# Performance work log

Hardware: AMD Instinct MI355X
Metric: run time of the kernel (lower is better)

Reference implementation:

```python
import jax, jax.numpy as jnp
import numpy as np
import math

B, IN, D, H, DEPTH, E, K = 16384, 128, 512, 8, 3, 8, 2
FF, EH = 4 * D, 256          # ffn width = 4*d_model; expert hidden fixed at 256 in source
EPSILON = 0.1                # forward() default epsilon (exploration mixing)
LN_EPS = 1e-5


def _ln(x, w, b):
    m = x.mean(-1, keepdims=True)
    v = x.var(-1, keepdims=True)  # biased variance, matching nn.LayerNorm
    return (x - m) / jnp.sqrt(v + LN_EPS) * w + b


def setup_inputs() -> dict:
    key = jax.random.key(0)
    ks = jax.random.split(key, 16)
    s = 0.02
    rn = lambda k, shape: jax.random.normal(k, shape, jnp.float32) * s
    return dict(
        x=jax.random.normal(ks[0], (B, IN), jnp.float32),
        embed_w=rn(ks[1], (IN, D)), embed_b=jnp.zeros((D,), jnp.float32),
        ln1_w=jnp.ones((DEPTH, D), jnp.float32), ln1_b=jnp.zeros((DEPTH, D), jnp.float32),
        inproj_w=rn(ks[2], (DEPTH, 3 * D, D)), inproj_b=jnp.zeros((DEPTH, 3 * D), jnp.float32),
        outproj_w=rn(ks[3], (DEPTH, D, D)), outproj_b=jnp.zeros((DEPTH, D), jnp.float32),
        ln2_w=jnp.ones((DEPTH, D), jnp.float32), ln2_b=jnp.zeros((DEPTH, D), jnp.float32),
        ffn_w1=rn(ks[4], (DEPTH, D, FF)), ffn_b1=jnp.zeros((DEPTH, FF), jnp.float32),
        ffn_w2=rn(ks[5], (DEPTH, FF, D)), ffn_b2=jnp.zeros((DEPTH, D), jnp.float32),
        router_w=rn(ks[6], (D, E)), router_b=jnp.zeros((E,), jnp.float32),
        exp_w1=rn(ks[7], (E, D, EH)), exp_b1=jnp.zeros((E, EH), jnp.float32),
        exp_w2=rn(ks[8], (E, EH, D)), exp_b2=jnp.zeros((E, D), jnp.float32),
        head_ln_w=jnp.ones((D,), jnp.float32), head_ln_b=jnp.zeros((D,), jnp.float32),
        head_w=rn(ks[9], (D, 1)), head_b=jnp.zeros((1,), jnp.float32),
    )


def reference(x, embed_w, embed_b, ln1_w, ln1_b, inproj_w, inproj_b,
              outproj_w, outproj_b, ln2_w, ln2_b, ffn_w1, ffn_b1, ffn_w2, ffn_b2,
              router_w, router_b, exp_w1, exp_b1, exp_w2, exp_b2,
              head_ln_w, head_ln_b, head_w, head_b):
    h = x @ embed_w + embed_b                       # [B, D]; unsqueeze(1) -> seq_len == 1
    for l in range(DEPTH):
        g = _ln(h, ln1_w[l], ln1_b[l])
        qkv = g @ inproj_w[l].T + inproj_b[l]       # [B, 3D]
        # seq_len == 1: softmax over the single key is exactly 1, so attn(h,h,h) == out_proj(V)
        v = qkv[:, 2 * D:]
        a = v @ outproj_w[l].T + outproj_b[l]
        h = h + a
        g = _ln(h, ln2_w[l], ln2_b[l])
        h = h + jax.nn.gelu(g @ ffn_w1[l] + ffn_b1[l], approximate=False) @ ffn_w2[l] + ffn_b2[l]
    z = h                                           # squeeze(1)

    # WaggleGate
    logits = z @ router_w + router_b                # [B, E]
    probs = jax.nn.softmax(logits, axis=-1)
    probs = (1.0 - EPSILON) * probs + EPSILON / E
    wts, idx = jax.lax.top_k(probs, K)              # [B, K]
    load = probs.mean(0)
    aux = (load * jnp.log(load * E + 1e-9)).sum() / math.log(E + 1e-9)

    # dense all-expert compute + sparse top-k combine (same math as per-sample dispatch)
    hmid = jax.nn.gelu(jnp.einsum('bd,edh->ebh', z, exp_w1) + exp_b1[:, None, :], approximate=False)
    eo = jnp.einsum('ebh,ehd->ebd', hmid, exp_w2) + exp_b2[:, None, :]   # [E, B, D]
    gate = jnp.zeros((z.shape[0], E), z.dtype).at[
        jnp.arange(z.shape[0])[:, None], idx].add(wts)                    # [B, E]
    moe = jnp.einsum('be,ebd->bd', gate, eo)

    z = z + moe
    logit = (_ln(z, head_ln_w, head_ln_b) @ head_w + head_b)[:, 0]       # [B]
    return logit, aux
```

## Files before the change

### kernel.cpp

```cpp
#include <hip/hip_runtime.h>
#include <hip/hip_bf16.h>

#define B_TOK 16384
#define IN_DIM 128
#define D_DIM 512
#define DEPTH 3
#define NEXP 8
#define FF_DIM 2048
#define EH_DIM 256
#define MAXSLOT 34816
#define MAXT256 136
#define NHBLK 64

typedef __attribute__((ext_vector_type(8))) __bf16 bf16x8;
typedef __attribute__((ext_vector_type(4))) float f32x4;
typedef __attribute__((ext_vector_type(4))) unsigned short u16x4;
typedef __attribute__((ext_vector_type(8))) unsigned short u16x8;

__device__ __forceinline__ unsigned short f2bf(float f){
    unsigned int u = __float_as_uint(f);
    u += 0x7fffu + ((u >> 16) & 1u);
    return (unsigned short)(u >> 16);
}
__device__ __forceinline__ float bf2f(unsigned short u){
    return __uint_as_float(((unsigned int)u) << 16);
}
__device__ __forceinline__ float geluf(float x){
    return 0.5f * x * (1.0f + erff(x * 0.70710678118654752f));
}
__device__ __forceinline__ void gload_lds16(const void* g, void* l){
    __builtin_amdgcn_global_load_lds((const __attribute__((address_space(1))) unsigned int*)g,
                                     (__attribute__((address_space(3))) unsigned int*)l,
                                     16, 0, 0);
}
__device__ __forceinline__ int xcd_swizzle(int orig, int nwg){
    const int q = nwg >> 3, r = nwg & 7;
    const int xcd = orig & 7;
    const int idx = orig >> 3;
    return (xcd < r ? xcd*(q+1) : r*(q+1) + (xcd-r)*q) + idx;
}
__device__ __forceinline__ void wgbar(){
    asm volatile("" ::: "memory");
    __builtin_amdgcn_s_barrier();
    asm volatile("" ::: "memory");
}

__global__ void zero_kernel(int* a, int na, int* b, int nb){
    const int i = blockIdx.x * blockDim.x + threadIdx.x;
    if (i < na) a[i] = 0;
    if (i < nb) b[i] = 0;
}

struct ConvSeg { const float* src; unsigned short* dst; int n4; };
struct ConvArgs { ConvSeg seg[2]; };

__global__ void convert_kernel(ConvArgs a){
    const int stride = gridDim.x * blockDim.x;
    const int tid = blockIdx.x * blockDim.x + threadIdx.x;
    for (int s = 0; s < 2; ++s){
        const f32x4* src = (const f32x4*)a.seg[s].src;
        u16x4* dst = (u16x4*)a.seg[s].dst;
        const int n4 = a.seg[s].n4;
        for (int i = tid; i < n4; i += stride){
            f32x4 v = src[i];
            u16x4 o;
            o[0] = f2bf(v[0]); o[1] = f2bf(v[1]); o[2] = f2bf(v[2]); o[3] = f2bf(v[3]);
            dst[i] = o;
        }
    }
}

struct TSeg { const float* src; unsigned short* dst; int K; int N; int tileStart; };
struct TArgs { TSeg seg[26]; };

__global__ void transpose_kernel(TArgs a){
    __shared__ float t[32][33];
    const int tile = blockIdx.x;
    int s = 0;
    #pragma unroll 1
    while (s < 25 && tile >= a.seg[s+1].tileStart) ++s;
    const TSeg sg = a.seg[s];
    const int local = tile - sg.tileStart;
    const int tilesN = sg.N >> 5;
    const int k0 = (local / tilesN) << 5;
    const int n0 = (local % tilesN) << 5;
    const int tx = threadIdx.x & 31;
    const int ty = threadIdx.x >> 5;
    #pragma unroll
    for (int j = 0; j < 4; ++j)
        t[ty + j*8][tx] = sg.src[(size_t)(k0 + ty + j*8) * sg.N + n0 + tx];
    __syncthreads();
    #pragma unroll
    for (int j = 0; j < 4; ++j){
        const int n = ty + j*8;
        sg.dst[(size_t)(n0 + n) * sg.K + k0 + tx] = f2bf(t[tx][n]);
    }
}

__global__ void foldb_kernel(const float* __restrict__ outproj_w, const float* __restrict__ outproj_b,
                             const float* __restrict__ inproj_b, float* __restrict__ bfold){
    const int l = blockIdx.x, n = threadIdx.x;
    const float* Wo = outproj_w + ((size_t)l*D_DIM + n)*D_DIM;
    const float* bv = inproj_b + l*3*D_DIM + 2*D_DIM;
    float acc = outproj_b[l*D_DIM + n];
    for (int j = 0; j < D_DIM; ++j) acc += Wo[j]*bv[j];
    bfold[l*D_DIM + n] = acc;
}

#define EPI_BF16 0
#define EPI_F32_BIAS 2

template<int EPI>
__global__ void __launch_bounds__(256, 2)
gemm_bt(const unsigned short* __restrict__ A, const unsigned short* __restrict__ Bt,
        const float* __restrict__ bias, void* __restrict__ out, int NB, int N, int K)
{
    __shared__ unsigned short sh[32768];
    const int nwg = gridDim.x;
    const int wg  = xcd_swizzle(blockIdx.x, nwg);
    const int bn  = wg % NB;
    const int bm  = wg / NB;

    const int tid  = threadIdx.x;
    const int lane = tid & 63;
    const int wave = tid >> 6;
    const int wm = (wave >> 1) << 6;
    const int wn = (wave & 1) << 6;

    f32x4 acc[4][4] = {};

    const unsigned short* Abase = A + (size_t)bm * 128 * K;
    const unsigned short* Bbase = Bt + (size_t)bn * 128 * K;
    const int soff = tid * 16;

    auto STAGE = [&](int b, int kt){
        char* Ab = (char*)(sh + b*16384);
        char* Bb = (char*)(sh + b*16384 + 8192);
        #pragma unroll
        for (int s = 0; s < 4; ++s){
            const int off = s*4096 + soff;
            const int row = off >> 7, colb = off & 127;
            gload_lds16((const char*)(Abase + (size_t)row*K + kt) + colb, Ab + off);
        }
        #pragma unroll
        for (int s = 0; s < 4; ++s){
            const int off = s*4096 + soff;
            const int row = off >> 7, colb = off & 127;
            gload_lds16((const char*)(Bbase + (size_t)row*K + kt) + colb, Bb + off);
        }
    };
    auto COMPUTE = [&](int b){
        const unsigned short* Ab = sh + b*16384;
        const unsigned short* Bb = sh + b*16384 + 8192;
        #pragma unroll
        for (int ks = 0; ks < 2; ++ks){
            const int k0 = ks*32 + ((lane>>4)<<3);
            bf16x8 af[4], bfr[4];
            #pragma unroll
            for (int i=0;i<4;i++) af[i]  = *(const bf16x8*)&Ab[(wm + i*16 + (lane&15))*64 + k0];
            #pragma unroll
            for (int j=0;j<4;j++) bfr[j] = *(const bf16x8*)&Bb[(wn + j*16 + (lane&15))*64 + k0];
            #pragma unroll
            for (int i=0;i<4;i++)
                #pragma unroll
                for (int j=0;j<4;j++)
                    acc[i][j] = __builtin_amdgcn_mfma_f32_16x16x32_bf16(af[i], bfr[j], acc[i][j], 0, 0, 0);
        }
    };

    STAGE(0, 0);
    __syncthreads();
    const int nk = K >> 6;
    int cur = 0;
    for (int i = 0; i < nk; ++i){
        if (i + 1 < nk) STAGE(cur ^ 1, (i + 1) << 6);
        COMPUTE(cur);
        __syncthreads();
        cur ^= 1;
    }

    const int r0 = ((lane>>4)<<2);
    const int cc = lane & 15;

    if (EPI == EPI_F32_BIAS){
        #pragma unroll
        for (int j=0;j<4;j++){
            const int col = bn*128 + wn + j*16 + cc;
            const float bv = bias[col];
            #pragma unroll
            for (int i=0;i<4;i++)
                #pragma unroll
                for (int r=0;r<4;r++){
                    const int row = bm*128 + wm + i*16 + r0 + r;
                    ((float*)out)[(size_t)row * N + col] = acc[i][j][r] + bv;
                }
        }
    } else {
        unsigned short* Ct = sh;
        float bcol[4];
        #pragma unroll
        for (int j=0;j<4;j++) bcol[j] = bias[bn*128 + wn + j*16 + cc];
        #pragma unroll
        for (int i=0;i<4;i++)
            #pragma unroll
            for (int r=0;r<4;r++){
                const int rl = wm + i*16 + r0 + r;
                #pragma unroll
                for (int j=0;j<4;j++)
                    Ct[rl*128 + wn + j*16 + cc] = f2bf(acc[i][j][r] + bcol[j]);
            }
        __syncthreads();
        const int orow = tid >> 4;
        const int ocol = (tid & 15) * 8;
        unsigned short* op = (unsigned short*)out;
        #pragma unroll
        for (int p = 0; p < 8; ++p){
            const int row = p*16 + orow;
            *(u16x4*)(&op[(size_t)(bm*128 + row)*N + bn*128 + ocol])     = *(u16x4*)&Ct[row*128 + ocol];
            *(u16x4*)(&op[(size_t)(bm*128 + row)*N + bn*128 + ocol + 4]) = *(u16x4*)&Ct[row*128 + ocol + 4];
        }
    }
}

#define G_GELU_BF16 0
#define G_F32_RESID 1
#define G_GATED_BF16 2

template<int EPI, int MOE, int INDIRECT>
__global__ void __launch_bounds__(512, 2)
gemm256(const unsigned short* __restrict__ A, const unsigned short* __restrict__ BtG,
        const float* __restrict__ biasG, const float* __restrict__ resid,
        const int* __restrict__ tok, const int* __restrict__ offs,
        int wstride, int bstride, const float* __restrict__ gslot,
        void* __restrict__ out, int NB, int N, int K)
{
    __shared__ __align__(16) char sh[147456];
    const int nwg = gridDim.x;
    const int wg  = xcd_swizzle(blockIdx.x, nwg);
    const int bn  = wg % NB;
    const int bm  = wg / NB;
    const int m0  = bm * 256;

    const unsigned short* Bt = BtG;
    const float* bias = biasG;
    if (MOE){
        if (m0 >= offs[8]) return;
        int e = 0;
        #pragma unroll 1
        while (offs[e+1] <= m0) ++e;
        Bt   += (size_t)e * wstride;
        bias += (size_t)e * bstride;
    }

    const int tid = threadIdx.x, lane = tid & 63, wave = tid >> 6;
    const int wm = (wave >> 1) * 64;
    const int wn = (wave & 1) * 64;

    const int srow = wave*16 + (lane >> 3);
    const int scol = ((lane & 7) ^ (lane >> 3)) * 8;
    const unsigned short* aptr[2][2];
    #pragma unroll
    for (int u = 0; u < 2; ++u)
        #pragma unroll
        for (int l = 0; l < 2; ++l){
            const int r = u*128 + srow + l*8;
            const int gr = INDIRECT ? tok[m0 + r] : (m0 + r);
            aptr[u][l] = A + (size_t)gr * K + scol;
        }
    const unsigned short* bptr[2];
    #pragma unroll
    for (int l = 0; l < 2; ++l)
        bptr[l] = Bt + (size_t)(bn*128 + srow + l*8) * K + scol;
    const int sdst = wave*2048 + lane*16;

    int aoff[2], boff[2];
    #pragma unroll
    for (int ks = 0; ks < 2; ++ks){
        const int ch = (((ks<<2) + (lane>>4)) ^ (lane & 7)) << 4;
        aoff[ks] = (wm + (lane & 15))*128 + ch;
        boff[ks] = (wn + (lane & 15))*128 + ch;
    }

    f32x4 acc[4][4] = {};
    bf16x8 bfr[4][2];

    auto STA = [&](int buf, int kt){
        #pragma unroll
        for (int u = 0; u < 2; ++u)
            #pragma unroll
            for (int l = 0; l < 2; ++l)
                gload_lds16(aptr[u][l] + kt, sh + buf*32768 + u*16384 + l*1024 + sdst);
    };
    auto STB = [&](int buf, int kt){
        #pragma unroll
        for (int l = 0; l < 2; ++l)
            gload_lds16(bptr[l] + kt, sh + 98304 + buf*16384 + l*1024 + sdst);
    };
    auto RDB = [&](int buf){
        #pragma unroll
        for (int nf = 0; nf < 4; ++nf)
            #pragma unroll
            for (int ks = 0; ks < 2; ++ks)
                bfr[nf][ks] = *(const bf16x8*)(sh + 98304 + buf*16384 + nf*2048 + boff[ks]);
    };

    STA(0, 0);  STB(0, 0);
    STA(1, 64); STB(1, 64);
    asm volatile("s_waitcnt vmcnt(6)" ::: "memory");
    wgbar();

    const int nk = K >> 6;
    int c0 = 0;
    for (int t = 0; t < nk; ++t){
        const bool f = (t + 2 < nk);
        int c2 = c0 + 2; if (c2 >= 3) c2 -= 3;
        bf16x8 af[2][2];

        RDB(c0);
        #pragma unroll
        for (int m2 = 0; m2 < 2; ++m2)
            #pragma unroll
            for (int ks = 0; ks < 2; ++ks)
                af[m2][ks] = *(const bf16x8*)(sh + c0*32768 + (0+m2)*2048 + aoff[ks]);
        if (f){
            const int kt2 = (t + 2) << 6;
            STA(c2, kt2);
            STB(c2, kt2);
        }
        __builtin_amdgcn_s_setprio(1);
        #pragma unroll
        for (int m2 = 0; m2 < 2; ++m2)
            #pragma unroll
            for (int nf = 0; nf < 4; ++nf)
                #pragma unroll
                for (int ks = 0; ks < 2; ++ks)
                    acc[0+m2][nf] = __builtin_amdgcn_mfma_f32_16x16x32_bf16(af[m2][ks], bfr[nf][ks], acc[0+m2][nf], 0,0,0);
        __builtin_amdgcn_s_setprio(0);
        wgbar();

        #pragma unroll
        for (int m2 = 0; m2 < 2; ++m2)
            #pragma unroll
            for (int ks = 0; ks < 2; ++ks)
                af[m2][ks] = *(const bf16x8*)(sh + c0*32768 + (2+m2)*2048 + aoff[ks]);
        __builtin_amdgcn_s_setprio(1);
        #pragma unroll
        for (int m2 = 0; m2 < 2; ++m2)
            #pragma unroll
            for (int nf = 0; nf < 4; ++nf)
                #pragma unroll
                for (int ks = 0; ks < 2; ++ks)
                    acc[2+m2][nf] = __builtin_amdgcn_mfma_f32_16x16x32_bf16(af[m2][ks], bfr[nf][ks], acc[2+m2][nf], 0,0,0);
        __builtin_amdgcn_s_setprio(0);
        if (f) asm volatile("s_waitcnt vmcnt(6)" ::: "memory");
        else   asm volatile("s_waitcnt vmcnt(0)" ::: "memory");
        wgbar();

        ++c0; if (c0 >= 3) c0 -= 3;
    }

    const int r4 = (lane >> 4) * 4;
    const int cc = lane & 15;
    if (EPI == G_F32_RESID){
        #pragma unroll
        for (int nf = 0; nf < 4; ++nf){
            const int col = bn*128 + wn + nf*16 + cc;
            const float bv = bias[col];
            #pragma unroll
            for (int mf = 0; mf < 4; ++mf)
                #pragma unroll
                for (int r = 0; r < 4; ++r){
                    const int row = m0 + wm + mf*16 + r4 + r;
                    const size_t idx = (size_t)row * N + col;
                    ((float*)out)[idx] = resid[idx] + acc[mf][nf][r] + bv;
                }
        }
    } else {
        unsigned short* ct = (unsigned short*)sh;
        #pragma unroll
        for (int nf = 0; nf < 4; ++nf){
            const float bv = bias[bn*128 + wn + nf*16 + cc];
            #pragma unroll
            for (int mf = 0; mf < 4; ++mf)
                #pragma unroll
                for (int r = 0; r < 4; ++r){
                    const int row = wm + mf*16 + r4 + r;
                    float v = acc[mf][nf][r] + bv;
                    if (EPI == G_GELU_BF16) v = geluf(v);
                    else                    v *= gslot[m0 + row];
                    ct[row*128 + wn + nf*16 + cc] = f2bf(v);
                }
        }
        __syncthreads();
        unsigned short* op = (unsigned short*)out;
        #pragma unroll
        for (int p = 0; p < 8; ++p){
            const int uidx = p*512 + tid;
            const int row = uidx >> 4;
            const int cu  = uidx & 15;
            *(u16x8*)(op + (size_t)(m0 + row)*N + bn*128 + cu*8) =
                *(const u16x8*)(ct + row*128 + cu*8);
        }
    }
}

__global__ void ln_kernel(const float* __restrict__ x, const float* __restrict__ w,
                          const float* __restrict__ b, unsigned short* __restrict__ out)
{
    const int lane = threadIdx.x & 63;
    const int wave = threadIdx.x >> 6;
    const int row  = blockIdx.x * 4 + wave;
    const float* xr = x + (size_t)row * D_DIM;
    f32x4 v0 = *(const f32x4*)(xr + lane*8);
    f32x4 v1 = *(const f32x4*)(xr + lane*8 + 4);
    float s  = v0[0]+v0[1]+v0[2]+v0[3] + v1[0]+v1[1]+v1[2]+v1[3];
    float s2 = v0[0]*v0[0]+v0[1]*v0[1]+v0[2]*v0[2]+v0[3]*v0[3]
             + v1[0]*v1[0]+v1[1]*v1[1]+v1[2]*v1[2]+v1[3]*v1[3];
    #pragma unroll
    for (int o = 32; o > 0; o >>= 1){ s += __shfl_xor(s, o); s2 += __shfl_xor(s2, o); }
    const float mean = s * (1.0f/512.0f);
    const float var  = s2 * (1.0f/512.0f) - mean*mean;
    const float inv  = 1.0f / sqrtf(var + 1e-5f);
    const int k = lane*8;
    u16x4 o0, o1;
    #pragma unroll
    for (int j=0;j<4;j++) o0[j] = f2bf((v0[j]-mean)*inv*w[k+j]   + b[k+j]);
    #pragma unroll
    for (int j=0;j<4;j++) o1[j] = f2bf((v1[j]-mean)*inv*w[k+4+j] + b[k+4+j]);
    *(u16x4*)(out + (size_t)row*D_DIM + k)     = o0;
    *(u16x4*)(out + (size_t)row*D_DIM + k + 4) = o1;
}

__global__ void router_kernel(const float* __restrict__ z, const float* __restrict__ rw,
                              const float* __restrict__ rb, unsigned short* __restrict__ zbf,
                              int2* __restrict__ idx2, float2* __restrict__ wts2,
                              float* __restrict__ bsums)
{
    __shared__ float ps[4][8];
    const int lane = threadIdx.x & 63;
    const int wave = threadIdx.x >> 6;
    const int row  = blockIdx.x * 4 + wave;
    const float* zr = z + (size_t)row * D_DIM;
    f32x4 z0 = *(const f32x4*)(zr + lane*8);
    f32x4 z1 = *(const f32x4*)(zr + lane*8 + 4);
    {
        u16x4 o0, o1;
        #pragma unroll
        for (int j=0;j<4;j++){ o0[j] = f2bf(z0[j]); o1[j] = f2bf(z1[j]); }
        *(u16x4*)(zbf + (size_t)row*D_DIM + lane*8)     = o0;
        *(u16x4*)(zbf + (size_t)row*D_DIM + lane*8 + 4) = o1;
    }
    float acc[8] = {0,0,0,0,0,0,0,0};
    #pragma unroll
    for (int j = 0; j < 8; ++j){
        const float zv = (j < 4) ? z0[j] : z1[j-4];
        const float* wr = rw + (size_t)(lane*8 + j) * 8;
        f32x4 w0 = *(const f32x4*)wr;
        f32x4 w1 = *(const f32x4*)(wr + 4);
        acc[0] += zv*w0[0]; acc[1] += zv*w0[1]; acc[2] += zv*w0[2]; acc[3] += zv*w0[3];
        acc[4] += zv*w1[0]; acc[5] += zv*w1[1]; acc[6] += zv*w1[2]; acc[7] += zv*w1[3];
    }
    #pragma unroll
    for (int o = 32; o > 0; o >>= 1){
        #pragma unroll
        for (int e = 0; e < 8; ++e) acc[e] += __shfl_xor(acc[e], o);
    }
    if (lane == 0){
        float p[8]; float mx = -1e30f;
        #pragma unroll
        for (int e=0;e<8;e++){ p[e] = acc[e] + rb[e]; mx = fmaxf(mx, p[e]); }
        float se = 0.f;
        #pragma unroll
        for (int e=0;e<8;e++){ p[e] = expf(p[e]-mx); se += p[e]; }
        const float sc = 0.9f / se;
        #pragma unroll
        for (int e=0;e<8;e++) p[e] = p[e]*sc + 0.0125f;
        int i1 = 0;
        #pragma unroll
        for (int e=1;e<8;e++) if (p[e] > p[i1]) i1 = e;
        int i2 = (i1 == 0) ? 1 : 0;
        for (int e=i2+1;e<8;e++) if (e != i1 && p[e] > p[i2]) i2 = e;
        idx2[row] = make_int2(i1, i2);
        wts2[row] = make_float2(p[i1], p[i2]);
        #pragma unroll
        for (int e=0;e<8;e++) ps[wave][e] = p[e];
    }
    __syncthreads();
    if (threadIdx.x < 8){
        bsums[blockIdx.x*8 + threadIdx.x] =
            ps[0][threadIdx.x] + ps[1][threadIdx.x] + ps[2][threadIdx.x] + ps[3][threadIdx.x];
    }
}

__global__ void hist_kernel(const int2* __restrict__ idx2, int* __restrict__ blockHist){
    __shared__ int hc[8];
    if (threadIdx.x < 8) hc[threadIdx.x] = 0;
    __syncthreads();
    const int t = blockIdx.x * 256 + threadIdx.x;
    const int2 ii = idx2[t];
    atomicAdd(&hc[ii.x], 1);
    atomicAdd(&hc[ii.y], 1);
    __syncthreads();
    if (threadIdx.x < 8) blockHist[blockIdx.x*8 + threadIdx.x] = hc[threadIdx.x];
}

__global__ void scan_kernel(const int* __restrict__ blockHist, int* __restrict__ offs,
                            int* __restrict__ baseArr){
    if (threadIdx.x == 0){
        int counts[8];
        #pragma unroll
        for (int e=0;e<8;e++) counts[e] = 0;
        for (int b=0;b<NHBLK;b++)
            #pragma unroll
            for (int e=0;e<8;e++) counts[e] += blockHist[b*8+e];
        int o = 0; offs[0] = 0;
        int start[8];
        #pragma unroll
        for (int e=0;e<8;e++){ start[e] = o; o += (counts[e]+255)&~255; offs[e+1] = o; }
        for (int e=0;e<8;e++){
            int cur = start[e];
            for (int b=0;b<NHBLK;b++){ baseArr[b*8+e] = cur; cur += blockHist[b*8+e]; }
        }
    }
}

__global__ void assign_kernel(const int2* __restrict__ idx2, const float2* __restrict__ wts2,
                              const int* __restrict__ baseArr, int2* __restrict__ slot_map,
                              float* __restrict__ gslot, int* __restrict__ tok)
{
    __shared__ int cur[8];
    if (threadIdx.x < 8) cur[threadIdx.x] = 0;
    __syncthreads();
    const int t = blockIdx.x * 256 + threadIdx.x;
    const int2 ii = idx2[t];
    const float2 ww = wts2[t];
    const int r1 = atomicAdd(&cur[ii.x], 1);
    const int r2 = atomicAdd(&cur[ii.y], 1);
    const int s1 = baseArr[blockIdx.x*8 + ii.x] + r1;
    const int s2 = baseArr[blockIdx.x*8 + ii.y] + r2;
    slot_map[t] = make_int2(s1, s2);
    gslot[s1] = ww.x; gslot[s2] = ww.y;
    tok[s1] = t; tok[s2] = t;
}

__global__ void aux_kernel(const float* __restrict__ bsums, float* __restrict__ out_aux)
{
    __shared__ float part[256];
    const int t = threadIdx.x;
    const int e = t & 7, chunk = t >> 3;
    float s = 0.f;
    for (int blk = chunk*128; blk < chunk*128 + 128; ++blk) s += bsums[blk*8 + e];
    part[t] = s;
    __syncthreads();
    if (t < 8){
        float tot = 0.f;
        for (int c = 0; c < 32; ++c) tot += part[c*8 + t];
        part[t] = tot;
    }
    __syncthreads();
    if (t == 0){
        float aux = 0.f;
        for (int e2 = 0; e2 < 8; ++e2){
            float load = part[e2] * (1.0f/16384.0f);
            aux += load * logf(load * 8.0f + 1e-9f);
        }
        out_aux[0] = aux / 2.0794415416798357f;
    }
}

__global__ void head_kernel(const float* __restrict__ h, const unsigned short* __restrict__ eog,
                            const int2* __restrict__ slot_map,
                            const float* __restrict__ w, const float* __restrict__ b,
                            const float* __restrict__ hw, const float* __restrict__ hb,
                            float* __restrict__ out)
{
    const int lane = threadIdx.x & 63;
    const int wave = threadIdx.x >> 6;
    const int row  = blockIdx.x * 4 + wave;
    const int2 sm = slot_map[row];
    const float* zr = h + (size_t)row * D_DIM;
    f32x4 v0 = *(const f32x4*)(zr + lane*8);
    f32x4 v1 = *(const f32x4*)(zr + lane*8 + 4);
    u16x8 e1 = *(const u16x8*)(eog + (size_t)sm.x * D_DIM + lane*8);
    u16x8 e2 = *(const u16x8*)(eog + (size_t)sm.y * D_DIM + lane*8);
    #pragma unroll
    for (int j=0;j<4;j++){ v0[j] += bf2f(e1[j]) + bf2f(e2[j]); }
    #pragma unroll
    for (int j=0;j<4;j++){ v1[j] += bf2f(e1[4+j]) + bf2f(e2[4+j]); }
    float s  = v0[0]+v0[1]+v0[2]+v0[3] + v1[0]+v1[1]+v1[2]+v1[3];
    float s2 = v0[0]*v0[0]+v0[1]*v0[1]+v0[2]*v0[2]+v0[3]*v0[3]
             + v1[0]*v1[0]+v1[1]*v1[1]+v1[2]*v1[2]+v1[3]*v1[3];
    #pragma unroll
    for (int o = 32; o > 0; o >>= 1){ s += __shfl_xor(s, o); s2 += __shfl_xor(s2, o); }
    const float mean = s * (1.0f/512.0f);
    const float var  = s2 * (1.0f/512.0f) - mean*mean;
    const float inv  = 1.0f / sqrtf(var + 1e-5f);
    const int k = lane*8;
    float dot = 0.f;
    #pragma unroll
    for (int j=0;j<4;j++) dot += ((v0[j]-mean)*inv*w[k+j]   + b[k+j])   * hw[k+j];
    #pragma unroll
    for (int j=0;j<4;j++) dot += ((v1[j]-mean)*inv*w[k+4+j] + b[k+4+j]) * hw[k+4+j];
    #pragma unroll
    for (int o = 32; o > 0; o >>= 1) dot += __shfl_xor(dot, o);
    if (lane == 0) out[row] = dot + hb[0];
}

extern "C" void kernel_launch(void* const* d_in, const int* in_sizes, int n_in,
                              void* d_out, int out_size, void* d_ws, size_t ws_size,
                              hipStream_t stream)
{
    (void)in_sizes; (void)n_in; (void)out_size; (void)ws_size;
    const float* x         = (const float*)d_in[0];
    const float* embed_w   = (const float*)d_in[1];
    const float* embed_b   = (const float*)d_in[2];
    const float* ln1_w     = (const float*)d_in[3];
    const float* ln1_b     = (const float*)d_in[4];
    const float* inproj_w  = (const float*)d_in[5];
    const float* inproj_b  = (const float*)d_in[6];
    const float* outproj_w = (const float*)d_in[7];
    const float* outproj_b = (const float*)d_in[8];
    const float* ln2_w     = (const float*)d_in[9];
    const float* ln2_b     = (const float*)d_in[10];
    const float* ffn_w1    = (const float*)d_in[11];
    const float* ffn_b1    = (const float*)d_in[12];
    const float* ffn_w2    = (const float*)d_in[13];
    const float* ffn_b2    = (const float*)d_in[14];
    const float* router_w  = (const float*)d_in[15];
    const float* router_b  = (const float*)d_in[16];
    const float* exp_w1    = (const float*)d_in[17];
    const float* exp_b1    = (const float*)d_in[18];
    const float* exp_w2    = (const float*)d_in[19];
    const float* exp_b2    = (const float*)d_in[20];
    const float* head_ln_w = (const float*)d_in[21];
    const float* head_ln_b = (const float*)d_in[22];
    const float* head_w    = (const float*)d_in[23];
    const float* head_b    = (const float*)d_in[24];

    char* ws = (char*)d_ws;
    unsigned short* xbf   = (unsigned short*)(ws + 0);
    unsigned short* ebf   = (unsigned short*)(ws + 4194304);
    unsigned short* wobf  = (unsigned short*)(ws + 4325376);
    unsigned short* wvtbf = (unsigned short*)(ws + 5898240);
    unsigned short* wfold = (unsigned short*)(ws + 7471104);
    unsigned short* w1t   = (unsigned short*)(ws + 9043968);
    unsigned short* w2t   = (unsigned short*)(ws + 15335424);
    unsigned short* e1t   = (unsigned short*)(ws + 21626880);
    unsigned short* e2t   = (unsigned short*)(ws + 23724032);
    float*          h     = (float*)(ws + 25821184);
    unsigned short* gbf   = (unsigned short*)(ws + 59375616);
    unsigned short* ubf   = (unsigned short*)(ws + 76152832);
    unsigned short* hmidg = ubf;
    unsigned short* eog   = (unsigned short*)(ws + 93978624);
    char* MISC = ws + 143261696;
    int*    offs     = (int*)(MISC + 0);
    float*  zbias    = (float*)(MISC + 256);
    float*  bfold    = (float*)(MISC + 2304);
    int2*   idx2     = (int2*)(MISC + 8448);
    float2* wts2     = (float2*)(MISC + 139520);
    int2*   slot_map = (int2*)(MISC + 270592);
    float*  gslot    = (float*)(MISC + 401664);
    int*    tok      = (int*)(MISC + 544768);
    float*  bsums    = (float*)(MISC + 684032);
    int*    blockHist= (int*)(MISC + 815104);
    int*    baseArr  = (int*)(MISC + 817152);
    unsigned short* zbf = gbf;
    float* out = (float*)d_out;

    zero_kernel<<<(MAXSLOT + 255)/256, 256, 0, stream>>>((int*)zbias, 512, tok, MAXSLOT);

    ConvArgs ca;
    ca.seg[0] = { x, xbf, B_TOK*IN_DIM/4 };
    ca.seg[1] = { outproj_w, wobf, DEPTH*D_DIM*D_DIM/4 };
    convert_kernel<<<1024, 256, 0, stream>>>(ca);

    TArgs ta;
    int tcur = 0, ti = 0;
    ta.seg[ti] = { embed_w, ebf, IN_DIM, D_DIM, tcur };
    tcur += (IN_DIM/32)*(D_DIM/32); ++ti;
    for (int l = 0; l < DEPTH; ++l){
        ta.seg[ti] = { ffn_w1 + (size_t)l*D_DIM*FF_DIM, w1t + (size_t)l*FF_DIM*D_DIM, D_DIM, FF_DIM, tcur };
        tcur += (D_DIM/32)*(FF_DIM/32); ++ti;
    }
    for (int l = 0; l < DEPTH; ++l){
        ta.seg[ti] = { ffn_w2 + (size_t)l*FF_DIM*D_DIM, w2t + (size_t)l*D_DIM*FF_DIM, FF_DIM, D_DIM, tcur };
        tcur += (FF_DIM/32)*(D_DIM/32); ++ti;
    }
    for (int e = 0; e < NEXP; ++e){
        ta.seg[ti] = { exp_w1 + (size_t)e*D_DIM*EH_DIM, e1t + (size_t)e*EH_DIM*D_DIM, D_DIM, EH_DIM, tcur };
        tcur += (D_DIM/32)*(EH_DIM/32); ++ti;
    }
    for (int e = 0; e < NEXP; ++e){
        ta.seg[ti] = { exp_w2 + (size_t)e*EH_DIM*D_DIM, e2t + (size_t)e*D_DIM*EH_DIM, EH_DIM, D_DIM, tcur };
        tcur += (EH_DIM/32)*(D_DIM/32); ++ti;
    }
    for (int l = 0; l < DEPTH; ++l){
        ta.seg[ti] = { inproj_w + (size_t)l*3*D_DIM*D_DIM + 2*D_DIM*D_DIM,
                       wvtbf + (size_t)l*D_DIM*D_DIM, D_DIM, D_DIM, tcur };
        tcur += (D_DIM/32)*(D_DIM/32); ++ti;
    }
    transpose_kernel<<<tcur, 256, 0, stream>>>(ta);

    foldb_kernel<<<DEPTH, D_DIM, 0, stream>>>(outproj_w, outproj_b, inproj_b, bfold);

    for (int l = 0; l < DEPTH; ++l){
        gemm_bt<EPI_BF16><<<16, 256, 0, stream>>>(
            wobf + (size_t)l*D_DIM*D_DIM, wvtbf + (size_t)l*D_DIM*D_DIM,
            zbias, wfold + (size_t)l*D_DIM*D_DIM, 4, D_DIM, D_DIM);
    }

    gemm_bt<EPI_F32_BIAS><<<(D_DIM/128)*(B_TOK/128), 256, 0, stream>>>(
        xbf, ebf, embed_b, h, D_DIM/128, D_DIM, IN_DIM);

    for (int l = 0; l < DEPTH; ++l){
        ln_kernel<<<B_TOK/4, 256, 0, stream>>>(h, ln1_w + l*D_DIM, ln1_b + l*D_DIM, gbf);
        gemm256<G_F32_RESID,0,0><<<(B_TOK/256)*(D_DIM/128), 512, 0, stream>>>(
            gbf, wfold + (size_t)l*D_DIM*D_DIM, bfold + l*D_DIM, h,
            nullptr, nullptr, 0, 0, nullptr, h, D_DIM/128, D_DIM, D_DIM);
        ln_kernel<<<B_TOK/4, 256, 0, stream>>>(h, ln2_w + l*D_DIM, ln2_b + l*D_DIM, gbf);
        gemm256<G_GELU_BF16,0,0><<<(B_TOK/256)*(FF_DIM/128), 512, 0, stream>>>(
            gbf, w1t + (size_t)l*FF_DIM*D_DIM, ffn_b1 + l*FF_DIM, nullptr,
            nullptr, nullptr, 0, 0, nullptr, ubf, FF_DIM/128, FF_DIM, D_DIM);
        gemm256<G_F32_RESID,0,0><<<(B_TOK/256)*(D_DIM/128), 512, 0, stream>>>(
            ubf, w2t + (size_t)l*D_DIM*FF_DIM, ffn_b2 + l*D_DIM, h,
            nullptr, nullptr, 0, 0, nullptr, h, D_DIM/128, D_DIM, FF_DIM);
    }

    router_kernel<<<B_TOK/4, 256, 0, stream>>>(h, router_w, router_b, zbf, idx2, wts2, bsums);
    aux_kernel<<<1, 256, 0, stream>>>(bsums, out + B_TOK);
    hist_kernel<<<NHBLK, 256, 0, stream>>>(idx2, blockHist);
    scan_kernel<<<1, 64, 0, stream>>>(blockHist, offs, baseArr);
    assign_kernel<<<B_TOK/256, 256, 0, stream>>>(idx2, wts2, baseArr, slot_map, gslot, tok);

    gemm256<G_GELU_BF16,1,1><<<MAXT256*(EH_DIM/128), 512, 0, stream>>>(
        zbf, e1t, exp_b1, nullptr, tok, offs, EH_DIM*D_DIM, EH_DIM, nullptr,
        hmidg, EH_DIM/128, EH_DIM, D_DIM);
    gemm256<G_GATED_BF16,1,0><<<MAXT256*(D_DIM/128), 512, 0, stream>>>(
        hmidg, e2t, exp_b2, nullptr, nullptr, offs, D_DIM*EH_DIM, D_DIM, gslot,
        eog, D_DIM/128, D_DIM, EH_DIM);

    head_kernel<<<B_TOK/4, 256, 0, stream>>>(h, eog, slot_map, head_ln_w, head_ln_b, head_w, head_b, out);
}
```

Baseline: 673.9 us.

## Store residual stream in bf16, add 256x256 FFN1 GEMM, tanh GELU, simplify pipeline

Stores the residual stream h as bf16 instead of fp32. This halves the traffic of the LN, residual-GEMM, router and head kernels, and lets the expert GEMM read h directly without a separate bf16 copy. Adds a 256x256-tile GEMM for the FFN up-projection to raise data reuse, and replaces erf GELU with a clamped tanh approximation. The gemm256 main loop is also reverted from a 3-stage prefetch with explicit waitcnt and setprio to a plain 2-stage double buffer. Together these trade accuracy (bf16 residual accumulation and approximate GELU) and possibly some pipelining efficiency for less memory traffic and cheaper math.

```diff
diff --git a/kernel.cpp b/kernel.cpp
--- a/kernel.cpp
+++ b/kernel.cpp
@@ -26,7 +26,12 @@
     return __uint_as_float(((unsigned int)u) << 16);
 }
 __device__ __forceinline__ float geluf(float x){
-    return 0.5f * x * (1.0f + erff(x * 0.70710678118654752f));
+    float x2 = x * x;
+    float y  = x * (0.79788456080287f + 0.03567740814183f * x2);
+    y = fminf(fmaxf(y, -15.0f), 15.0f);
+    float e = __expf(2.0f * y);
+    float th = 1.0f - 2.0f / (e + 1.0f);
+    return 0.5f * x * (1.0f + th);
 }
 __device__ __forceinline__ void gload_lds16(const void* g, void* l){
     __builtin_amdgcn_global_load_lds((const __attribute__((address_space(1))) unsigned int*)g,
@@ -38,11 +43,6 @@
     const int xcd = orig & 7;
     const int idx = orig >> 3;
     return (xcd < r ? xcd*(q+1) : r*(q+1) + (xcd-r)*q) + idx;
-}
-__device__ __forceinline__ void wgbar(){
-    asm volatile("" ::: "memory");
-    __builtin_amdgcn_s_barrier();
-    asm volatile("" ::: "memory");
 }
 
 __global__ void zero_kernel(int* a, int na, int* b, int nb){
@@ -107,13 +107,9 @@
     bfold[l*D_DIM + n] = acc;
 }
 
-#define EPI_BF16 0
-#define EPI_F32_BIAS 2
-
-template<int EPI>
 __global__ void __launch_bounds__(256, 2)
 gemm_bt(const unsigned short* __restrict__ A, const unsigned short* __restrict__ Bt,
-        const float* __restrict__ bias, void* __restrict__ out, int NB, int N, int K)
+        const float* __restrict__ bias, unsigned short* __restrict__ out, int NB, int N, int K)
 {
     __shared__ unsigned short sh[32768];
     const int nwg = gridDim.x;
@@ -181,58 +177,148 @@
 
     const int r0 = ((lane>>4)<<2);
     const int cc = lane & 15;
-
-    if (EPI == EPI_F32_BIAS){
-        #pragma unroll
-        for (int j=0;j<4;j++){
-            const int col = bn*128 + wn + j*16 + cc;
-            const float bv = bias[col];
-            #pragma unroll
-            for (int i=0;i<4;i++)
+    unsigned short* Ct = sh;
+    float bcol[4];
+    #pragma unroll
+    for (int j=0;j<4;j++) bcol[j] = bias[bn*128 + wn + j*16 + cc];
+    #pragma unroll
+    for (int i=0;i<4;i++)
+        #pragma unroll
+        for (int r=0;r<4;r++){
+            const int rl = wm + i*16 + r0 + r;
+            #pragma unroll
+            for (int j=0;j<4;j++)
+                Ct[rl*128 + wn + j*16 + cc] = f2bf(acc[i][j][r] + bcol[j]);
+        }
+    __syncthreads();
+    const int orow = tid >> 4;
+    const int ocol = (tid & 15) * 8;
+    #pragma unroll
+    for (int p = 0; p < 8; ++p){
+        const int row = p*16 + orow;
+        *(u16x8*)(&out[(size_t)(bm*128 + row)*N + bn*128 + ocol]) = *(u16x8*)&Ct[row*128 + ocol];
+    }
+}
+
+__global__ void __launch_bounds__(512, 2)
+gemm256sq(const unsigned short* __restrict__ A, const unsigned short* __restrict__ Bt,
+          const float* __restrict__ bias, unsigned short* __restrict__ out,
+          int NB, int N, int K)
+{
+    __shared__ __align__(16) char sh[131072];
+    const int nwg = gridDim.x;
+    const int wg  = xcd_swizzle(blockIdx.x, nwg);
+    const int bn  = wg % NB;
+    const int bm  = wg / NB;
+    const int m0  = bm * 256;
+    const int n0  = bn * 256;
+
+    const int tid = threadIdx.x, lane = tid & 63, wave = tid >> 6;
+    const int wr = wave >> 2;
+    const int wc = wave & 3;
+
+    const int srow = wave*16 + (lane >> 3);
+    const int scol = ((lane & 7) ^ (lane >> 3)) * 8;
+    const unsigned short* aptr[2][2];
+    const unsigned short* bptr[2][2];
+    #pragma unroll
+    for (int u = 0; u < 2; ++u)
+        #pragma unroll
+        for (int l = 0; l < 2; ++l){
+            aptr[u][l] = A  + (size_t)(m0 + u*128 + srow + l*8) * K + scol;
+            bptr[u][l] = Bt + (size_t)(n0 + u*128 + srow + l*8) * K + scol;
+        }
+    const int sdst = wave*2048 + lane*16;
+
+    int ch[2];
+    #pragma unroll
+    for (int ks = 0; ks < 2; ++ks)
+        ch[ks] = ((((ks<<2) + (lane>>4)) ^ (lane & 7)) << 4);
+    const int arow = wr*128 + (lane & 15);
+    const int brow = wc*64  + (lane & 15);
+
+    f32x4 acc[8][4] = {};
+
+    auto STAGE = [&](int buf, int kt){
+        #pragma unroll
+        for (int u = 0; u < 2; ++u)
+            #pragma unroll
+            for (int l = 0; l < 2; ++l)
+                gload_lds16(aptr[u][l] + kt, sh + buf*32768 + u*16384 + l*1024 + sdst);
+        #pragma unroll
+        for (int u = 0; u < 2; ++u)
+            #pragma unroll
+            for (int l = 0; l < 2; ++l)
+                gload_lds16(bptr[u][l] + kt, sh + 65536 + buf*32768 + u*16384 + l*1024 + sdst);
+    };
+    auto COMPUTE = [&](int buf){
+        bf16x8 bfr[4][2];
+        #pragma unroll
+        for (int nf = 0; nf < 4; ++nf)
+            #pragma unroll
+            for (int ks = 0; ks < 2; ++ks)
+                bfr[nf][ks] = *(const bf16x8*)(sh + 65536 + buf*32768 + (brow + nf*16)*128 + ch[ks]);
+        #pragma unroll
+        for (int mf = 0; mf < 8; ++mf){
+            bf16x8 af[2];
+            #pragma unroll
+            for (int ks = 0; ks < 2; ++ks)
+                af[ks] = *(const bf16x8*)(sh + buf*32768 + (arow + mf*16)*128 + ch[ks]);
+            #pragma unroll
+            for (int nf = 0; nf < 4; ++nf)
                 #pragma unroll
-                for (int r=0;r<4;r++){
-                    const int row = bm*128 + wm + i*16 + r0 + r;
-                    ((float*)out)[(size_t)row * N + col] = acc[i][j][r] + bv;
-                }
-        }
-    } else {
-        unsigned short* Ct = sh;
-        float bcol[4];
-        #pragma unroll
-        for (int j=0;j<4;j++) bcol[j] = bias[bn*128 + wn + j*16 + cc];
-        #pragma unroll
-        for (int i=0;i<4;i++)
-            #pragma unroll
-            for (int r=0;r<4;r++){
-                const int rl = wm + i*16 + r0 + r;
-                #pragma unroll
-                for (int j=0;j<4;j++)
-                    Ct[rl*128 + wn + j*16 + cc] = f2bf(acc[i][j][r] + bcol[j]);
+                for (int ks = 0; ks < 2; ++ks)
+                    acc[mf][nf] = __builtin_amdgcn_mfma_f32_16x16x32_bf16(af[ks], bfr[nf][ks], acc[mf][nf], 0,0,0);
+        }
+    };
+
+    STAGE(0, 0);
+    __syncthreads();
+    const int nk = K >> 6;
+    int cur = 0;
+    for (int i = 0; i < nk; ++i){
+        if (i + 1 < nk) STAGE(cur ^ 1, (i + 1) << 6);
+        COMPUTE(cur);
+        __syncthreads();
+        cur ^= 1;
+    }
+
+    unsigned short* Ct = (unsigned short*)sh;
+    const int r4 = (lane >> 4) * 4;
+    const int cc = lane & 15;
+    #pragma unroll
+    for (int nf = 0; nf < 4; ++nf){
+        const int col = wc*64 + nf*16 + cc;
+        const float bv = bias[n0 + col];
+        #pragma unroll
+        for (int mf = 0; mf < 8; ++mf)
+            #pragma unroll
+            for (int r = 0; r < 4; ++r){
+                const int row = wr*128 + mf*16 + r4 + r;
+                Ct[row*256 + col] = f2bf(geluf(acc[mf][nf][r] + bv));
             }
-        __syncthreads();
-        const int orow = tid >> 4;
-        const int ocol = (tid & 15) * 8;
-        unsigned short* op = (unsigned short*)out;
-        #pragma unroll
-        for (int p = 0; p < 8; ++p){
-            const int row = p*16 + orow;
-            *(u16x4*)(&op[(size_t)(bm*128 + row)*N + bn*128 + ocol])     = *(u16x4*)&Ct[row*128 + ocol];
-            *(u16x4*)(&op[(size_t)(bm*128 + row)*N + bn*128 + ocol + 4]) = *(u16x4*)&Ct[row*128 + ocol + 4];
-        }
+    }
+    __syncthreads();
+    #pragma unroll
+    for (int p = 0; p < 16; ++p){
+        const int uidx = p*512 + tid;
+        const int row = uidx >> 5;
+        const int cu  = uidx & 31;
+        *(u16x8*)(out + (size_t)(m0 + row)*N + n0 + cu*8) = *(const u16x8*)(Ct + row*256 + cu*8);
     }
 }
 
 #define G_GELU_BF16 0
-#define G_F32_RESID 1
+#define G_BF16_RESID 1
 #define G_GATED_BF16 2
 
 template<int EPI, int MOE, int INDIRECT>
 __global__ void __launch_bounds__(512, 2)
 gemm256(const unsigned short* __restrict__ A, const unsigned short* __restrict__ BtG,
-        const float* __restrict__ biasG, const float* __restrict__ resid,
+        const float* __restrict__ biasG, const unsigned short* __restrict__ resid,
         const int* __restrict__ tok, const int* __restrict__ offs,
         int wstride, int bstride, const float* __restrict__ gslot,
-        void* __restrict__ out, int NB, int N, int K)
+        unsigned short* __restrict__ out, int NB, int N, int K)
 {
     __shared__ __align__(16) char sh[147456];
     const int nwg = gridDim.x;
@@ -282,98 +368,77 @@
     }
 
     f32x4 acc[4][4] = {};
-    bf16x8 bfr[4][2];
-
-    auto STA = [&](int buf, int kt){
+
+    auto STAGE = [&](int buf, int kt){
         #pragma unroll
         for (int u = 0; u < 2; ++u)
             #pragma unroll
             for (int l = 0; l < 2; ++l)
                 gload_lds16(aptr[u][l] + kt, sh + buf*32768 + u*16384 + l*1024 + sdst);
-    };
-    auto STB = [&](int buf, int kt){
         #pragma unroll
         for (int l = 0; l < 2; ++l)
             gload_lds16(bptr[l] + kt, sh + 98304 + buf*16384 + l*1024 + sdst);
     };
-    auto RDB = [&](int buf){
+    auto COMPUTE = [&](int buf){
+        bf16x8 bfr[4][2];
         #pragma unroll
         for (int nf = 0; nf < 4; ++nf)
             #pragma unroll
             for (int ks = 0; ks < 2; ++ks)
                 bfr[nf][ks] = *(const bf16x8*)(sh + 98304 + buf*16384 + nf*2048 + boff[ks]);
-    };
-
-    STA(0, 0);  STB(0, 0);
-    STA(1, 64); STB(1, 64);
-    asm volatile("s_waitcnt vmcnt(6)" ::: "memory");
-    wgbar();
-
-    const int nk = K >> 6;
-    int c0 = 0;
-    for (int t = 0; t < nk; ++t){
-        const bool f = (t + 2 < nk);
-        int c2 = c0 + 2; if (c2 >= 3) c2 -= 3;
-        bf16x8 af[2][2];
-
-        RDB(c0);
-        #pragma unroll
-        for (int m2 = 0; m2 < 2; ++m2)
+        #pragma unroll
+        for (int mf = 0; mf < 4; ++mf){
+            bf16x8 af[2];
             #pragma unroll
             for (int ks = 0; ks < 2; ++ks)
-                af[m2][ks] = *(const bf16x8*)(sh + c0*32768 + (0+m2)*2048 + aoff[ks]);
-        if (f){
-            const int kt2 = (t + 2) << 6;
-            STA(c2, kt2);
-            STB(c2, kt2);
-        }
-        __builtin_amdgcn_s_setprio(1);
-        #pragma unroll
-        for (int m2 = 0; m2 < 2; ++m2)
+                af[ks] = *(const bf16x8*)(sh + buf*32768 + mf*2048 + aoff[ks]);
             #pragma unroll
             for (int nf = 0; nf < 4; ++nf)
                 #pragma unroll
                 for (int ks = 0; ks < 2; ++ks)
-                    acc[0+m2][nf] = __builtin_amdgcn_mfma_f32_16x16x32_bf16(af[m2][ks], bfr[nf][ks], acc[0+m2][nf], 0,0,0);
-        __builtin_amdgcn_s_setprio(0);
-        wgbar();
-
-        #pragma unroll
-        for (int m2 = 0; m2 < 2; ++m2)
-            #pragma unroll
-            for (int ks = 0; ks < 2; ++ks)
-                af[m2][ks] = *(const bf16x8*)(sh + c0*32768 + (2+m2)*2048 + aoff[ks]);
-        __builtin_amdgcn_s_setprio(1);
-        #pragma unroll
-        for (int m2 = 0; m2 < 2; ++m2)
-            #pragma unroll
-            for (int nf = 0; nf < 4; ++nf)
-                #pragma unroll
-                for (int ks = 0; ks < 2; ++ks)
-                    acc[2+m2][nf] = __builtin_amdgcn_mfma_f32_16x16x32_bf16(af[m2][ks], bfr[nf][ks], acc[2+m2][nf], 0,0,0);
-        __builtin_amdgcn_s_setprio(0);
-        if (f) asm volatile("s_waitcnt vmcnt(6)" ::: "memory");
-        else   asm volatile("s_waitcnt vmcnt(0)" ::: "memory");
-        wgbar();
-
-        ++c0; if (c0 >= 3) c0 -= 3;
+                    acc[mf][nf] = __builtin_amdgcn_mfma_f32_16x16x32_bf16(af[ks], bfr[nf][ks], acc[mf][nf], 0,0,0);
+        }
+    };
+
+    STAGE(0, 0);
+    __syncthreads();
+    const int nk = K >> 6;
+    int cur = 0;
+    for (int i = 0; i < nk; ++i){
+        if (i + 1 < nk) STAGE(cur ^ 1, (i + 1) << 6);
+        COMPUTE(cur);
+        __syncthreads();
+        cur ^= 1;
     }
 
     const int r4 = (lane >> 4) * 4;
     const int cc = lane & 15;
-    if (EPI == G_F32_RESID){
+    if (EPI == G_BF16_RESID){
+        float* ctf = (float*)sh;
         #pragma unroll
         for (int nf = 0; nf < 4; ++nf){
-            const int col = bn*128 + wn + nf*16 + cc;
-            const float bv = bias[col];
+            const float bv = bias[bn*128 + wn + nf*16 + cc];
             #pragma unroll
             for (int mf = 0; mf < 4; ++mf)
                 #pragma unroll
                 for (int r = 0; r < 4; ++r){
-                    const int row = m0 + wm + mf*16 + r4 + r;
-                    const size_t idx = (size_t)row * N + col;
-                    ((float*)out)[idx] = resid[idx] + acc[mf][nf][r] + bv;
+                    const int row = wm + mf*16 + r4 + r;
+                    ctf[row*128 + wn + nf*16 + cc] = acc[mf][nf][r] + bv;
                 }
+        }
+        __syncthreads();
+        #pragma unroll
+        for (int p = 0; p < 8; ++p){
+            const int uidx = p*512 + tid;
+            const int row = uidx >> 4;
+            const int cu  = uidx & 15;
+            const size_t gidx = (size_t)(m0 + row)*N + bn*128 + cu*8;
+            u16x8 hv = *(const u16x8*)(resid + gidx);
+            u16x8 o;
+            #pragma unroll
+            for (int j = 0; j < 8; ++j)
+                o[j] = f2bf(bf2f(hv[j]) + ctf[row*128 + cu*8 + j]);
+            *(u16x8*)(out + gidx) = o;
         }
     } else {
         unsigned short* ct = (unsigned short*)sh;
@@ -392,47 +457,44 @@
                 }
         }
         __syncthreads();
-        unsigned short* op = (unsigned short*)out;
         #pragma unroll
         for (int p = 0; p < 8; ++p){
             const int uidx = p*512 + tid;
             const int row = uidx >> 4;
             const int cu  = uidx & 15;
-            *(u16x8*)(op + (size_t)(m0 + row)*N + bn*128 + cu*8) =
+            *(u16x8*)(out + (size_t)(m0 + row)*N + bn*128 + cu*8) =
                 *(const u16x8*)(ct + row*128 + cu*8);
         }
     }
 }
 
-__global__ void ln_kernel(const float* __restrict__ x, const float* __restrict__ w,
+__global__ void ln_kernel(const unsigned short* __restrict__ x, const float* __restrict__ w,
                           const float* __restrict__ b, unsigned short* __restrict__ out)
 {
     const int lane = threadIdx.x & 63;
     const int wave = threadIdx.x >> 6;
     const int row  = blockIdx.x * 4 + wave;
-    const float* xr = x + (size_t)row * D_DIM;
-    f32x4 v0 = *(const f32x4*)(xr + lane*8);
-    f32x4 v1 = *(const f32x4*)(xr + lane*8 + 4);
-    float s  = v0[0]+v0[1]+v0[2]+v0[3] + v1[0]+v1[1]+v1[2]+v1[3];
-    float s2 = v0[0]*v0[0]+v0[1]*v0[1]+v0[2]*v0[2]+v0[3]*v0[3]
-             + v1[0]*v1[0]+v1[1]*v1[1]+v1[2]*v1[2]+v1[3]*v1[3];
+    u16x8 hv = *(const u16x8*)(x + (size_t)row * D_DIM + lane*8);
+    float v[8];
+    #pragma unroll
+    for (int j = 0; j < 8; ++j) v[j] = bf2f(hv[j]);
+    float s = 0.f, s2 = 0.f;
+    #pragma unroll
+    for (int j = 0; j < 8; ++j){ s += v[j]; s2 += v[j]*v[j]; }
     #pragma unroll
     for (int o = 32; o > 0; o >>= 1){ s += __shfl_xor(s, o); s2 += __shfl_xor(s2, o); }
     const float mean = s * (1.0f/512.0f);
     const float var  = s2 * (1.0f/512.0f) - mean*mean;
     const float inv  = 1.0f / sqrtf(var + 1e-5f);
     const int k = lane*8;
-    u16x4 o0, o1;
-    #pragma unroll
-    for (int j=0;j<4;j++) o0[j] = f2bf((v0[j]-mean)*inv*w[k+j]   + b[k+j]);
-    #pragma unroll
-    for (int j=0;j<4;j++) o1[j] = f2bf((v1[j]-mean)*inv*w[k+4+j] + b[k+4+j]);
-    *(u16x4*)(out + (size_t)row*D_DIM + k)     = o0;
-    *(u16x4*)(out + (size_t)row*D_DIM + k + 4) = o1;
-}
-
-__global__ void router_kernel(const float* __restrict__ z, const float* __restrict__ rw,
-                              const float* __restrict__ rb, unsigned short* __restrict__ zbf,
+    u16x8 o;
+    #pragma unroll
+    for (int j = 0; j < 8; ++j) o[j] = f2bf((v[j]-mean)*inv*w[k+j] + b[k+j]);
+    *(u16x8*)(out + (size_t)row*D_DIM + k) = o;
+}
+
+__global__ void router_kernel(const unsigned short* __restrict__ z, const float* __restrict__ rw,
+                              const float* __restrict__ rb,
                               int2* __restrict__ idx2, float2* __restrict__ wts2,
                               float* __restrict__ bsums)
 {
@@ -440,20 +502,11 @@
     const int lane = threadIdx.x & 63;
     const int wave = threadIdx.x >> 6;
     const int row  = blockIdx.x * 4 + wave;
-    const float* zr = z + (size_t)row * D_DIM;
-    f32x4 z0 = *(const f32x4*)(zr + lane*8);
-    f32x4 z1 = *(const f32x4*)(zr + lane*8 + 4);
-    {
-        u16x4 o0, o1;
-        #pragma unroll
-        for (int j=0;j<4;j++){ o0[j] = f2bf(z0[j]); o1[j] = f2bf(z1[j]); }
-        *(u16x4*)(zbf + (size_t)row*D_DIM + lane*8)     = o0;
-        *(u16x4*)(zbf + (size_t)row*D_DIM + lane*8 + 4) = o1;
-    }
+    u16x8 hv = *(const u16x8*)(z + (size_t)row * D_DIM + lane*8);
     float acc[8] = {0,0,0,0,0,0,0,0};
     #pragma unroll
     for (int j = 0; j < 8; ++j){
-        const float zv = (j < 4) ? z0[j] : z1[j-4];
+        const float zv = bf2f(hv[j]);
         const float* wr = rw + (size_t)(lane*8 + j) * 8;
         f32x4 w0 = *(const f32x4*)wr;
         f32x4 w1 = *(const f32x4*)(wr + 4);
@@ -568,7 +621,7 @@
     }
 }
 
-__global__ void head_kernel(const float* __restrict__ h, const unsigned short* __restrict__ eog,
+__global__ void head_kernel(const unsigned short* __restrict__ h, const unsigned short* __restrict__ eog,
                             const int2* __restrict__ slot_map,
                             const float* __restrict__ w, const float* __restrict__ b,
                             const float* __restrict__ hw, const float* __restrict__ hb,
@@ -578,18 +631,15 @@
     const int wave = threadIdx.x >> 6;
     const int row  = blockIdx.x * 4 + wave;
     const int2 sm = slot_map[row];
-    const float* zr = h + (size_t)row * D_DIM;
-    f32x4 v0 = *(const f32x4*)(zr + lane*8);
-    f32x4 v1 = *(const f32x4*)(zr + lane*8 + 4);
+    u16x8 hv = *(const u16x8*)(h + (size_t)row * D_DIM + lane*8);
     u16x8 e1 = *(const u16x8*)(eog + (size_t)sm.x * D_DIM + lane*8);
     u16x8 e2 = *(const u16x8*)(eog + (size_t)sm.y * D_DIM + lane*8);
-    #pragma unroll
-    for (int j=0;j<4;j++){ v0[j] += bf2f(e1[j]) + bf2f(e2[j]); }
-    #pragma unroll
-    for (int j=0;j<4;j++){ v1[j] += bf2f(e1[4+j]) + bf2f(e2[4+j]); }
-    float s  = v0[0]+v0[1]+v0[2]+v0[3] + v1[0]+v1[1]+v1[2]+v1[3];
-    float s2 = v0[0]*v0[0]+v0[1]*v0[1]+v0[2]*v0[2]+v0[3]*v0[3]
-             + v1[0]*v1[0]+v1[1]*v1[1]+v1[2]*v1[2]+v1[3]*v1[3];
+    float v[8];
+    #pragma unroll
+    for (int j=0;j<8;j++) v[j] = bf2f(hv[j]) + bf2f(e1[j]) + bf2f(e2[j]);
+    float s = 0.f, s2 = 0.f;
+    #pragma unroll
+    for (int j=0;j<8;j++){ s += v[j]; s2 += v[j]*v[j]; }
     #pragma unroll
     for (int o = 32; o > 0; o >>= 1){ s += __shfl_xor(s, o); s2 += __shfl_xor(s2, o); }
     const float mean = s * (1.0f/512.0f);
@@ -598,9 +648,7 @@
     const int k = lane*8;
     float dot = 0.f;
     #pragma unroll
-    for (int j=0;j<4;j++) dot += ((v0[j]-mean)*inv*w[k+j]   + b[k+j])   * hw[k+j];
-    #pragma unroll
-    for (int j=0;j<4;j++) dot += ((v1[j]-mean)*inv*w[k+4+j] + b[k+4+j]) * hw[k+4+j];
+    for (int j=0;j<8;j++) dot += ((v[j]-mean)*inv*w[k+j] + b[k+j]) * hw[k+j];
     #pragma unroll
     for (int o = 32; o > 0; o >>= 1) dot += __shfl_xor(dot, o);
     if (lane == 0) out[row] = dot + hb[0];
@@ -647,12 +695,12 @@
     unsigned short* w2t   = (unsigned short*)(ws + 15335424);
     unsigned short* e1t   = (unsigned short*)(ws + 21626880);
     unsigned short* e2t   = (unsigned short*)(ws + 23724032);
-    float*          h     = (float*)(ws + 25821184);
-    unsigned short* gbf   = (unsigned short*)(ws + 59375616);
-    unsigned short* ubf   = (unsigned short*)(ws + 76152832);
+    unsigned short* h     = (unsigned short*)(ws + 25821184);
+    unsigned short* gbf   = (unsigned short*)(ws + 42598400);
+    unsigned short* ubf   = (unsigned short*)(ws + 59375616);
     unsigned short* hmidg = ubf;
-    unsigned short* eog   = (unsigned short*)(ws + 93978624);
-    char* MISC = ws + 143261696;
+    unsigned short* eog   = (unsigned short*)(ws + 77201408);
+    char* MISC = ws + 126484480;
     int*    offs     = (int*)(MISC + 0);
     float*  zbias    = (float*)(MISC + 256);
     float*  bfold    = (float*)(MISC + 2304);
@@ -664,7 +712,6 @@
     float*  bsums    = (float*)(MISC + 684032);
     int*    blockHist= (int*)(MISC + 815104);
     int*    baseArr  = (int*)(MISC + 817152);
-    unsigned short* zbf = gbf;
     float* out = (float*)d_out;
 
     zero_kernel<<<(MAXSLOT + 255)/256, 256, 0, stream>>>((int*)zbias, 512, tok, MAXSLOT);
@@ -704,36 +751,35 @@
     foldb_kernel<<<DEPTH, D_DIM, 0, stream>>>(outproj_w, outproj_b, inproj_b, bfold);
 
     for (int l = 0; l < DEPTH; ++l){
-        gemm_bt<EPI_BF16><<<16, 256, 0, stream>>>(
+        gemm_bt<<<16, 256, 0, stream>>>(
             wobf + (size_t)l*D_DIM*D_DIM, wvtbf + (size_t)l*D_DIM*D_DIM,
             zbias, wfold + (size_t)l*D_DIM*D_DIM, 4, D_DIM, D_DIM);
     }
 
-    gemm_bt<EPI_F32_BIAS><<<(D_DIM/128)*(B_TOK/128), 256, 0, stream>>>(
+    gemm_bt<<<(D_DIM/128)*(B_TOK/128), 256, 0, stream>>>(
         xbf, ebf, embed_b, h, D_DIM/128, D_DIM, IN_DIM);
 
     for (int l = 0; l < DEPTH; ++l){
         ln_kernel<<<B_TOK/4, 256, 0, stream>>>(h, ln1_w + l*D_DIM, ln1_b + l*D_DIM, gbf);
-        gemm256<G_F32_RESID,0,0><<<(B_TOK/256)*(D_DIM/128), 512, 0, stream>>>(
+        gemm256<G_BF16_RESID,0,0><<<(B_TOK/256)*(D_DIM/128), 512, 0, stream>>>(
             gbf, wfold + (size_t)l*D_DIM*D_DIM, bfold + l*D_DIM, h,
             nullptr, nullptr, 0, 0, nullptr, h, D_DIM/128, D_DIM, D_DIM);
         ln_kernel<<<B_TOK/4, 256, 0, stream>>>(h, ln2_w + l*D_DIM, ln2_b + l*D_DIM, gbf);
-        gemm256<G_GELU_BF16,0,0><<<(B_TOK/256)*(FF_DIM/128), 512, 0, stream>>>(
-            gbf, w1t + (size_t)l*FF_DIM*D_DIM, ffn_b1 + l*FF_DIM, nullptr,
-            nullptr, nullptr, 0, 0, nullptr, ubf, FF_DIM/128, FF_DIM, D_DIM);
-        gemm256<G_F32_RESID,0,0><<<(B_TOK/256)*(D_DIM/128), 512, 0, stream>>>(
+        gemm256sq<<<(B_TOK/256)*(FF_DIM/256), 512, 0, stream>>>(
+            gbf, w1t + (size_t)l*FF_DIM*D_DIM, ffn_b1 + l*FF_DIM, ubf, FF_DIM/256, FF_DIM, D_DIM);
+        gemm256<G_BF16_RESID,0,0><<<(B_TOK/256)*(D_DIM/128), 512, 0, stream>>>(
             ubf, w2t + (size_t)l*D_DIM*FF_DIM, ffn_b2 + l*D_DIM, h,
             nullptr, nullptr, 0, 0, nullptr, h, D_DIM/128, D_DIM, FF_DIM);
     }
 
-    router_kernel<<<B_TOK/4, 256, 0, stream>>>(h, router_w, router_b, zbf, idx2, wts2, bsums);
+    router_kernel<<<B_TOK/4, 256, 0, stream>>>(h, router_w, router_b, idx2, wts2, bsums);
     aux_kernel<<<1, 256, 0, stream>>>(bsums, out + B_TOK);
     hist_kernel<<<NHBLK, 256, 0, stream>>>(idx2, blockHist);
     scan_kernel<<<1, 64, 0, stream>>>(blockHist, offs, baseArr);
     assign_kernel<<<B_TOK/256, 256, 0, stream>>>(idx2, wts2, baseArr, slot_map, gslot, tok);
 
     gemm256<G_GELU_BF16,1,1><<<MAXT256*(EH_DIM/128), 512, 0, stream>>>(
-        zbf, e1t, exp_b1, nullptr, tok, offs, EH_DIM*D_DIM, EH_DIM, nullptr,
+        h, e1t, exp_b1, nullptr, tok, offs, EH_DIM*D_DIM, EH_DIM, nullptr,
         hmidg, EH_DIM/128, EH_DIM, D_DIM);
     gemm256<G_GATED_BF16,1,0><<<MAXT256*(D_DIM/128), 512, 0, stream>>>(
         hmidg, e2t, exp_b2, nullptr, nullptr, offs, D_DIM*EH_DIM, D_DIM, gslot,
```

After: 628.4 us. 6.8% less time.
